# Performance work log

Measured on AMD Instinct MI355X. Metric: run time of the kernel, lower is better.

The kernel has to match this reference:

```python
import jax, jax.numpy as jnp
import numpy as np

EMBED = 64
HEAD = 16

def setup_inputs() -> dict:
    key = jax.random.key(0)
    k1, k2, k3, k4 = jax.random.split(key, 4)
    x = jax.random.normal(k1, (4, 4096, EMBED), dtype=jnp.float32)
    # store weights as [in, out] so forward is x @ W (equivalent to torch Linear with W.T)
    Wq = jax.random.normal(k2, (EMBED, HEAD), dtype=jnp.float32) * (1.0 / np.sqrt(EMBED))
    Wk = jax.random.normal(k3, (EMBED, HEAD), dtype=jnp.float32) * (1.0 / np.sqrt(EMBED))
    Wv = jax.random.normal(k4, (EMBED, EMBED), dtype=jnp.float32) * (1.0 / np.sqrt(EMBED))
    return {"x": x, "Wq": Wq, "Wk": Wk, "Wv": Wv}

def reference(x, Wq, Wk, Wv):
    # q,k: [B,T,HEAD]; v: [B,T,EMBED]
    q = x @ Wq
    k = x @ Wk
    v = x @ Wv
    scores = jnp.einsum('bqh,bkh->bqk', q, k)  # [B,T,T]
    T = scores.shape[-1]
    # causal mask: positions with key > query set to -inf BEFORE scaling (matches original; same result)
    causal = jnp.tril(jnp.ones((T, T), dtype=bool))
    scores = jnp.where(causal, scores, -jnp.inf)
    attn = jax.nn.softmax(scores / np.sqrt(HEAD).astype(np.float32), axis=-1)
    return jnp.einsum('bqk,bkd->bqd', attn, v)  # [B,T,EMBED]
```

## Files before the change

### kernel.cpp

```cpp
#include <hip/hip_runtime.h>


#define TSEQ 4096
#define NBATCH 4

typedef __attribute__((ext_vector_type(4)))  float fvec4;
typedef __attribute__((ext_vector_type(16))) float f32x16;
typedef __attribute__((ext_vector_type(4)))  short s16x4;
typedef __attribute__((ext_vector_type(8)))  short s16x8;

union I4S8 { int i[4]; s16x8 v; };

static __device__ __forceinline__ unsigned short f2bf(float f) {
    unsigned u = __float_as_uint(f);
    u += 0x7FFFu + ((u >> 16) & 1u);
    return (unsigned short)(u >> 16);
}

static __device__ __forceinline__ int cvt_pk_bf16(float lo, float hi) {
    int r;
    asm("v_cvt_pk_bf16_f32 %0, %1, %2" : "=v"(r) : "v"(lo), "v"(hi));
    return r;
}

static __device__ __forceinline__ s16x8 cat4(s16x4 a, s16x4 b) {
    return __builtin_shufflevector(a, b, 0, 1, 2, 3, 4, 5, 6, 7);
}

__global__ __launch_bounds__(1024)
__attribute__((amdgpu_waves_per_eu(4, 4)))
void proj_kernel(
    const float* __restrict__ x,  const float* __restrict__ Wq,
    const float* __restrict__ Wk, const float* __restrict__ Wv,
    unsigned short* __restrict__ qb, unsigned short* __restrict__ kb,
    unsigned short* __restrict__ vf)
{
    __shared__ float xs[64][66];
    __shared__ __align__(16) unsigned short Wh[96][76], Wl[96][76];

    const int bid  = blockIdx.x;
    const int tid  = threadIdx.x;
    const int w    = tid >> 6;
    const int lane = tid & 63;
    const int col  = lane & 31;
    const int g    = lane >> 5;

    {
        const float* xblk = x + (size_t)bid * 64 * 64;
        const int fi = tid * 4;
        fvec4 v = *(const fvec4*)(xblk + fi);
        const int r = fi >> 6, c = fi & 63;
        xs[r][c + 0] = v[0]; xs[r][c + 1] = v[1];
        xs[r][c + 2] = v[2]; xs[r][c + 3] = v[3];
    }
    const float SCQ = 0.25f * 1.44269504088896340736f;
    {
        const int n = tid & 15, k = tid >> 4;
        float wv = Wq[tid] * SCQ;
        unsigned short h = f2bf(wv);
        Wh[n][k] = h;
        Wl[n][k] = f2bf(wv - __uint_as_float((unsigned)h << 16));
    }
    {
        const int n = tid & 15, k = tid >> 4;
        float wv = Wk[tid];
        unsigned short h = f2bf(wv);
        Wh[16 + n][k] = h;
        Wl[16 + n][k] = f2bf(wv - __uint_as_float((unsigned)h << 16));
    }
    #pragma unroll
    for (int j = 0; j < 4; ++j) {
        const int idx = tid + 1024 * j;
        const int n = idx & 63, k = idx >> 6;
        float wv = Wv[idx];
        unsigned short h = f2bf(wv);
        Wh[32 + n][k] = h;
        Wl[32 + n][k] = f2bf(wv - __uint_as_float((unsigned)h << 16));
    }
    __syncthreads();

    if (w < 6) {
        const int nt = w >> 1;
        const int rh = w & 1;
        const int row0 = bid * 64 + rh * 32;
        const int lrow = rh * 32 + col;

        s16x8 xh[4], xl[4];
        #pragma unroll
        for (int kc = 0; kc < 4; ++kc) {
            const float* xp = &xs[lrow][kc * 16 + 8 * g];
            float2 a0 = *(const float2*)(xp + 0);
            float2 a1 = *(const float2*)(xp + 2);
            float2 a2 = *(const float2*)(xp + 4);
            float2 a3 = *(const float2*)(xp + 6);
            I4S8 uh, ul;
            uh.i[0] = cvt_pk_bf16(a0.x, a0.y);
            uh.i[1] = cvt_pk_bf16(a1.x, a1.y);
            uh.i[2] = cvt_pk_bf16(a2.x, a2.y);
            uh.i[3] = cvt_pk_bf16(a3.x, a3.y);
            ul.i[0] = cvt_pk_bf16(a0.x - __uint_as_float((unsigned)uh.i[0] << 16),
                                  a0.y - __uint_as_float((unsigned)uh.i[0] & 0xffff0000u));
            ul.i[1] = cvt_pk_bf16(a1.x - __uint_as_float((unsigned)uh.i[1] << 16),
                                  a1.y - __uint_as_float((unsigned)uh.i[1] & 0xffff0000u));
            ul.i[2] = cvt_pk_bf16(a2.x - __uint_as_float((unsigned)uh.i[2] << 16),
                                  a2.y - __uint_as_float((unsigned)uh.i[2] & 0xffff0000u));
            ul.i[3] = cvt_pk_bf16(a3.x - __uint_as_float((unsigned)uh.i[3] << 16),
                                  a3.y - __uint_as_float((unsigned)uh.i[3] & 0xffff0000u));
            xh[kc] = uh.v; xl[kc] = ul.v;
        }

        f32x16 acc = (f32x16)0.0f;
        const int n = nt * 32 + col;
        #pragma unroll
        for (int kc = 0; kc < 4; ++kc) {
            const int off = kc * 16 + 8 * g;
            s16x8 bh = cat4(*(const s16x4*)&Wh[n][off], *(const s16x4*)&Wh[n][off + 4]);
            s16x8 bl = cat4(*(const s16x4*)&Wl[n][off], *(const s16x4*)&Wl[n][off + 4]);
            acc = __builtin_amdgcn_mfma_f32_32x32x16_bf16(xh[kc], bh, acc, 0, 0, 0);
            acc = __builtin_amdgcn_mfma_f32_32x32x16_bf16(xl[kc], bh, acc, 0, 0, 0);
            acc = __builtin_amdgcn_mfma_f32_32x32x16_bf16(xh[kc], bl, acc, 0, 0, 0);
        }

        if (nt == 0) {
            unsigned short* dst = (col < 16) ? (qb + col) : (kb + (col - 16));
            #pragma unroll
            for (int rr = 0; rr < 16; ++rr) {
                const int grow = row0 + (rr & 3) + 8 * (rr >> 2) + 4 * g;
                dst[(size_t)grow * 16] = f2bf(acc[rr]);
            }
        } else {
            const int mt = nt - 1;
            unsigned short* const vtile = vf + (size_t)bid * 4096;
            #pragma unroll
            for (int ci = 0; ci < 2; ++ci) {
                I4S8 pk;
                pk.i[0] = cvt_pk_bf16(acc[8*ci + 0], acc[8*ci + 1]);
                pk.i[1] = cvt_pk_bf16(acc[8*ci + 2], acc[8*ci + 3]);
                pk.i[2] = cvt_pk_bf16(acc[8*ci + 4], acc[8*ci + 5]);
                pk.i[3] = cvt_pk_bf16(acc[8*ci + 6], acc[8*ci + 7]);
                const int c = 2 * rh + ci;
                *(s16x8*)(vtile + ((c * 2 + mt) * 64 + lane) * 8) = pk.v;
            }
        }
    }
}

template<bool DIAG>
static __device__ __forceinline__ void do_tile32(
    const unsigned short* kp, const unsigned short* vt, const int lane,
    const s16x8 qf, const s16x8 ones, const int col, const int g,
    f32x16& o0, f32x16& o1, f32x16& osum)
{
    s16x8 kf   = *(const s16x8*)(kp);
    s16x8 va00 = *(const s16x8*)(vt + (0 * 64 + lane) * 8);
    s16x8 va01 = *(const s16x8*)(vt + (1 * 64 + lane) * 8);
    s16x8 va10 = *(const s16x8*)(vt + (2 * 64 + lane) * 8);
    s16x8 va11 = *(const s16x8*)(vt + (3 * 64 + lane) * 8);

    f32x16 s = __builtin_amdgcn_mfma_f32_32x32x16_bf16(kf, qf, (f32x16)0.0f, 0, 0, 0);

    #pragma unroll
    for (int rr = 0; rr < 16; ++rr) {
        float ev = __builtin_amdgcn_exp2f(s[rr]);
        if (DIAG) {
            const int drow = (rr & 3) + 8 * (rr >> 2) + 4 * g;
            ev = (drow <= col) ? ev : 0.f;
        }
        s[rr] = ev;
    }

    I4S8 pa, pb;
    pa.i[0] = cvt_pk_bf16(s[0],  s[1]);
    pa.i[1] = cvt_pk_bf16(s[2],  s[3]);
    pa.i[2] = cvt_pk_bf16(s[4],  s[5]);
    pa.i[3] = cvt_pk_bf16(s[6],  s[7]);
    pb.i[0] = cvt_pk_bf16(s[8],  s[9]);
    pb.i[1] = cvt_pk_bf16(s[10], s[11]);
    pb.i[2] = cvt_pk_bf16(s[12], s[13]);
    pb.i[3] = cvt_pk_bf16(s[14], s[15]);

    o0   = __builtin_amdgcn_mfma_f32_32x32x16_bf16(va00, pa.v, o0,   0, 0, 0);
    o1   = __builtin_amdgcn_mfma_f32_32x32x16_bf16(va01, pa.v, o1,   0, 0, 0);
    osum = __builtin_amdgcn_mfma_f32_32x32x16_bf16(ones, pa.v, osum, 0, 0, 0);
    o0   = __builtin_amdgcn_mfma_f32_32x32x16_bf16(va10, pb.v, o0,   0, 0, 0);
    o1   = __builtin_amdgcn_mfma_f32_32x32x16_bf16(va11, pb.v, o1,   0, 0, 0);
    osum = __builtin_amdgcn_mfma_f32_32x32x16_bf16(ones, pb.v, osum, 0, 0, 0);
}

__global__ __launch_bounds__(1024)
__attribute__((amdgpu_num_vgpr(128), amdgpu_waves_per_eu(4, 4)))
void attn_kernel(
    const unsigned short* __restrict__ qb, const unsigned short* __restrict__ kb,
    const unsigned short* __restrict__ vf, float* __restrict__ out)
{
    __shared__ float pl[16][32];
    __shared__ float pO[2048 * 17];
    __shared__ float outS[32][66];

    const int tid  = threadIdx.x;
    const int w    = tid >> 6;
    const int lane = tid & 63;
    const int col  = lane & 31;
    const int g    = lane >> 5;
    const int b    = blockIdx.y;
    const int p    = blockIdx.x;

    I4S8 onesu;
    onesu.i[0] = 0x3F803F80; onesu.i[1] = 0x3F803F80;
    onesu.i[2] = 0x3F803F80; onesu.i[3] = 0x3F803F80;
    const s16x8 ones = onesu.v;

    const unsigned short* const kbase = kb + (size_t)b * TSEQ * 16 + (size_t)col * 16 + 8 * g;
    const unsigned short* const vbase = vf + (size_t)b * 64 * 4096;

    for (int half = 0; half < 2; ++half) {
        const int i  = half ? (127 - p) : p;
        const int q0 = i * 32;

        const s16x8 qf = *(const s16x8*)(qb + ((size_t)(b * TSEQ) + q0 + col) * 16 + 8 * g);

        f32x16 o0 = (f32x16)0.0f, o1 = (f32x16)0.0f, osum = (f32x16)0.0f;

        int t = w;
        for (; t < i; t += 16) {
            do_tile32<false>(kbase + (size_t)t * 512,
                             vbase + (size_t)(t >> 1) * 4096 + (t & 1) * 2048,
                             lane, qf, ones, col, g, o0, o1, osum);
        }
        if (t == i) {
            do_tile32<true>(kbase + (size_t)t * 512,
                            vbase + (size_t)(t >> 1) * 4096 + (t & 1) * 2048,
                            lane, qf, ones, col, g, o0, o1, osum);
        }

        if (g == 0) pl[w][col] = osum[0];
        #pragma unroll
        for (int mt = 0; mt < 2; ++mt) {
            const f32x16 oa = mt ? o1 : o0;
            #pragma unroll
            for (int rr = 0; rr < 16; ++rr) {
                const int dv = mt * 32 + (rr & 3) + 8 * (rr >> 2) + 4 * g;
                pO[(dv * 32 + col) * 17 + w] = oa[rr];
            }
        }
        __syncthreads();

        {
            const int q   = tid & 31;
            const int dvh = tid >> 5;
            float L = 0.f;
            #pragma unroll
            for (int ww = 0; ww < 16; ++ww) L += pl[ww][q];
            const float inv = 1.0f / L;
            #pragma unroll
            for (int pass = 0; pass < 2; ++pass) {
                const int dv = dvh + 32 * pass;
                const float* prow = &pO[(dv * 32 + q) * 17];
                float sA = 0.f, sB = 0.f;
                #pragma unroll
                for (int c = 0; c < 8; ++c) { sA += prow[2*c]; sB += prow[2*c+1]; }
                outS[q][dv] = (sA + sB) * inv;
            }
        }
        __syncthreads();

        {
            const int q2  = tid >> 5;
            const int dvp = (tid & 31) * 2;
            float2 v2 = *(const float2*)&outS[q2][dvp];
            *(float2*)(out + ((size_t)(b * TSEQ) + q0 + q2) * 64 + dvp) = v2;
        }
    }
}

extern "C" void kernel_launch(void* const* d_in, const int* in_sizes, int n_in,
                              void* d_out, int out_size, void* d_ws, size_t ws_size,
                              hipStream_t stream) {
    const float* x  = (const float*)d_in[0];
    const float* Wq = (const float*)d_in[1];
    const float* Wk = (const float*)d_in[2];
    const float* Wv = (const float*)d_in[3];

    unsigned short* qb = (unsigned short*)d_ws;
    unsigned short* kb = qb + (size_t)NBATCH * TSEQ * 16;
    unsigned short* vf = kb + (size_t)NBATCH * TSEQ * 16;
    float* out = (float*)d_out;

    proj_kernel<<<dim3((NBATCH * TSEQ) / 64), 1024, 0, stream>>>(x, Wq, Wk, Wv, qb, kb, vf);
    attn_kernel<<<dim3(64, NBATCH), 1024, 0, stream>>>(qb, kb, vf, out);
}
```

Measured before the change: 23.86 us.

## Pack partial outputs as bf16 pairs in LDS and strength-reduce tile pointers

The per-wave partial output accumulators are packed into bf16 pairs before being written to the cross-wave reduction buffer. This halves LDS usage and store count, and the reduction now reads one packed word per pair of output columns. Tile pointers are advanced incrementally instead of being recomputed each iteration, and the explicit VGPR cap is dropped. The bf16 rounding of partial sums adds numerical error to the output, and removing the register cap may change register allocation.

```diff
diff --git a/kernel.cpp b/kernel.cpp
--- a/kernel.cpp
+++ b/kernel.cpp
@@ -188,13 +188,13 @@
 }
 
 __global__ __launch_bounds__(1024)
-__attribute__((amdgpu_num_vgpr(128), amdgpu_waves_per_eu(4, 4)))
+__attribute__((amdgpu_waves_per_eu(4, 4)))
 void attn_kernel(
     const unsigned short* __restrict__ qb, const unsigned short* __restrict__ kb,
     const unsigned short* __restrict__ vf, float* __restrict__ out)
 {
     __shared__ float pl[16][32];
-    __shared__ float pO[2048 * 17];
+    __shared__ int   pOi[1024 * 17];
     __shared__ float outS[32][66];
 
     const int tid  = threadIdx.x;
@@ -211,7 +211,8 @@
     const s16x8 ones = onesu.v;
 
     const unsigned short* const kbase = kb + (size_t)b * TSEQ * 16 + (size_t)col * 16 + 8 * g;
-    const unsigned short* const vbase = vf + (size_t)b * 64 * 4096;
+    const unsigned short* const vbase = vf + (size_t)b * 64 * 4096
+                                      + (size_t)(w >> 1) * 4096 + (w & 1) * 2048;
 
     for (int half = 0; half < 2; ++half) {
         const int i  = half ? (127 - p) : p;
@@ -221,16 +222,15 @@
 
         f32x16 o0 = (f32x16)0.0f, o1 = (f32x16)0.0f, osum = (f32x16)0.0f;
 
+        const unsigned short* kp = kbase + (size_t)w * 512;
+        const unsigned short* vt = vbase;
         int t = w;
         for (; t < i; t += 16) {
-            do_tile32<false>(kbase + (size_t)t * 512,
-                             vbase + (size_t)(t >> 1) * 4096 + (t & 1) * 2048,
-                             lane, qf, ones, col, g, o0, o1, osum);
+            do_tile32<false>(kp, vt, lane, qf, ones, col, g, o0, o1, osum);
+            kp += 8192; vt += 32768;
         }
         if (t == i) {
-            do_tile32<true>(kbase + (size_t)t * 512,
-                            vbase + (size_t)(t >> 1) * 4096 + (t & 1) * 2048,
-                            lane, qf, ones, col, g, o0, o1, osum);
+            do_tile32<true>(kp, vt, lane, qf, ones, col, g, o0, o1, osum);
         }
 
         if (g == 0) pl[w][col] = osum[0];
@@ -238,37 +238,39 @@
         for (int mt = 0; mt < 2; ++mt) {
             const f32x16 oa = mt ? o1 : o0;
             #pragma unroll
-            for (int rr = 0; rr < 16; ++rr) {
-                const int dv = mt * 32 + (rr & 3) + 8 * (rr >> 2) + 4 * g;
-                pO[(dv * 32 + col) * 17 + w] = oa[rr];
+            for (int j = 0; j < 8; ++j) {
+                const int rr = 2 * j;
+                const int d0 = mt * 32 + (rr & 3) + 8 * (rr >> 2) + 4 * g;
+                pOi[((d0 >> 1) * 32 + col) * 17 + w] = cvt_pk_bf16(oa[rr], oa[rr + 1]);
             }
         }
         __syncthreads();
 
         {
             const int q   = tid & 31;
-            const int dvh = tid >> 5;
+            const int dvp = tid >> 5;
             float L = 0.f;
             #pragma unroll
             for (int ww = 0; ww < 16; ++ww) L += pl[ww][q];
             const float inv = 1.0f / L;
-            #pragma unroll
-            for (int pass = 0; pass < 2; ++pass) {
-                const int dv = dvh + 32 * pass;
-                const float* prow = &pO[(dv * 32 + q) * 17];
-                float sA = 0.f, sB = 0.f;
-                #pragma unroll
-                for (int c = 0; c < 8; ++c) { sA += prow[2*c]; sB += prow[2*c+1]; }
-                outS[q][dv] = (sA + sB) * inv;
-            }
+            const int* prow = &pOi[(dvp * 32 + q) * 17];
+            float sA = 0.f, sB = 0.f;
+            #pragma unroll
+            for (int c = 0; c < 16; ++c) {
+                const int v = prow[c];
+                sA += __uint_as_float((unsigned)v << 16);
+                sB += __uint_as_float((unsigned)v & 0xffff0000u);
+            }
+            outS[q][2 * dvp + 0] = sA * inv;
+            outS[q][2 * dvp + 1] = sB * inv;
         }
         __syncthreads();
 
         {
             const int q2  = tid >> 5;
-            const int dvp = (tid & 31) * 2;
-            float2 v2 = *(const float2*)&outS[q2][dvp];
-            *(float2*)(out + ((size_t)(b * TSEQ) + q0 + q2) * 64 + dvp) = v2;
+            const int dvq = (tid & 31) * 2;
+            float2 v2 = *(const float2*)&outS[q2][dvq];
+            *(float2*)(out + ((size_t)(b * TSEQ) + q0 + q2) * 64 + dvq) = v2;
         }
     }
 }
```

Result: faster. 23.21 us (-2.7%).
